# Performance work log

Measured on AMD Instinct MI355X. Metric: run time of the kernel, lower is better.

## Reference

```python
import jax, jax.numpy as jnp
import numpy as np

B, S, D, H = 2, 2048, 2048, 16
HD = D // H  # 128 head dim


def setup_inputs() -> dict:
    key = jax.random.key(0)
    k1, k2, k3 = jax.random.split(key, 3)
    x = jax.random.normal(k1, (B, S, D), dtype=jnp.float32)
    w_qkv = jax.random.normal(k2, (3 * D, D), dtype=jnp.float32) * 0.02
    w_out = jax.random.normal(k3, (D, D), dtype=jnp.float32) * 0.02
    # complex-like RoPE table: freqs_cis[s, j] = exp(i * s * theta^{-2j/hd})
    theta = 10000.0
    inv_freq = 1.0 / (theta ** (jnp.arange(0, HD, 2, dtype=jnp.float32) / HD))  # [HD/2]
    t = jnp.arange(S, dtype=jnp.float32)
    freqs = jnp.outer(t, inv_freq)  # [S, HD/2]
    return {"x": x, "w_qkv": w_qkv, "w_out": w_out,
            "freqs_cos": jnp.cos(freqs), "freqs_sin": jnp.sin(freqs)}


def _apply_rope(t, cos, sin):
    # t: [b, s, h, hd]; adjacent pairs treated as complex (real, imag)
    b, s, h, hd = t.shape
    tr = t.reshape(b, s, h, hd // 2, 2)
    re, im = tr[..., 0], tr[..., 1]
    c = cos[None, :, None, :]  # [1, s, 1, hd/2]
    sn = sin[None, :, None, :]
    out_re = re * c - im * sn
    out_im = re * sn + im * c
    return jnp.stack([out_re, out_im], axis=-1).reshape(b, s, h, hd)


def reference(x, w_qkv, w_out, freqs_cos, freqs_sin):
    b, s, d = x.shape
    qkv = x @ w_qkv.T  # [b, s, 3d]
    q, k, v = jnp.split(qkv, 3, axis=-1)
    q = q.reshape(b, s, H, HD)
    k = k.reshape(b, s, H, HD)
    v = v.reshape(b, s, H, HD)
    q = _apply_rope(q, freqs_cos, freqs_sin)
    k = _apply_rope(k, freqs_cos, freqs_sin)
    # causal SDPA
    scale = 1.0 / jnp.sqrt(jnp.asarray(HD, dtype=x.dtype))
    scores = jnp.einsum("bqhd,bkhd->bhqk", q, k) * scale  # [b, h, s, s]
    causal = jnp.tril(jnp.ones((s, s), dtype=bool))
    scores = jnp.where(causal[None, None], scores, jnp.finfo(scores.dtype).min)
    attn = jax.nn.softmax(scores, axis=-1)
    out = jnp.einsum("bhqk,bkhd->bqhd", attn, v).reshape(b, s, d)
    return out @ w_out.T
```

## Files before the change

### kernel.cpp

```cpp
#include <hip/hip_runtime.h>
#include <hip/hip_bf16.h>
#include <stdint.h>

#define S_ 2048
#define D_ 2048
#define H_ 16
#define HD_ 128

typedef __bf16 bf16x8 __attribute__((ext_vector_type(8)));
typedef float f32x4 __attribute__((ext_vector_type(4)));
typedef unsigned short ushort_t;
typedef ushort_t us4 __attribute__((ext_vector_type(4)));

__device__ __forceinline__ float bf2f(ushort_t u) {
  union { float f; uint32_t i; } x; x.i = ((uint32_t)u) << 16; return x.f;
}
__device__ __forceinline__ ushort_t f2bf(float f) {
  union { float f; uint32_t i; } x; x.f = f;
  uint32_t r = x.i + 0x7fffu + ((x.i >> 16) & 1u);
  return (ushort_t)(r >> 16);
}

__device__ __forceinline__ void async_copy16(const void* g, void* l) {
  __builtin_amdgcn_global_load_lds(
      (const __attribute__((address_space(1))) unsigned int*)g,
      (__attribute__((address_space(3))) unsigned int*)l, 16, 0, 0);
}

__device__ __forceinline__ void store_val(float* p, float v) { *p = v; }
__device__ __forceinline__ void store_val(ushort_t* p, float v) { *p = f2bf(v); }

__global__ __launch_bounds__(256) void cvt_f32_bf16(const float* __restrict__ in,
                                                    ushort_t* __restrict__ out,
                                                    int n4) {
  int i = blockIdx.x * 256 + threadIdx.x;
  if (i >= n4) return;
  const float4 v = ((const float4*)in)[i];
  us4 o;
  o.x = f2bf(v.x); o.y = f2bf(v.y); o.z = f2bf(v.z); o.w = f2bf(v.w);
  ((us4*)out)[i] = o;
}

__device__ __forceinline__ void stage_B32(const ushort_t* __restrict__ g, int K,
                                          ushort_t* l, int wave, int srow,
                                          int clog) {
  async_copy16(g + (size_t)srow * K + clog * 8, l + wave * 512);
  async_copy16(g + (size_t)(128 + srow) * K + clog * 8, l + 4096 + wave * 512);
}
__device__ __forceinline__ void stage_A32(const ushort_t* __restrict__ g, int K,
                                          ushort_t* l, int wave, int srow,
                                          int clog) {
  async_copy16(g + (size_t)srow * K + clog * 8, l + wave * 512);
}

#define MFMA_BF16(a, b, c) __builtin_amdgcn_mfma_f32_16x16x32_bf16(a, b, c, 0, 0, 0)

template <typename OutT>
__global__ __launch_bounds__(512, 4) void gemm_bt_occ2(const ushort_t* __restrict__ A,
                                                       const ushort_t* __restrict__ Bm,
                                                       OutT* __restrict__ C,
                                                       int M, int N, int K) {
  __shared__ __align__(16) ushort_t As[2][128 * 32];
  __shared__ __align__(16) ushort_t Bs[3][256 * 32];
  const int tid = threadIdx.x;
  const int wave = tid >> 6, lane = tid & 63;
  const int quad = lane >> 4, l16 = lane & 15;
  const int bm = blockIdx.y * 128, bn = blockIdx.x * 256;
  const int wm = (wave >> 2) * 64;
  const int wn = (wave & 3) * 64;
  const int srow = tid >> 2;
  const int clog = (tid & 3) ^ ((tid >> 3) & 3);
  const int ck = (quad ^ ((l16 >> 1) & 3)) * 8;

  const ushort_t* gA = A + (size_t)bm * K;
  const ushort_t* gB = Bm + (size_t)bn * K;
  const int NT = K >> 5;

  f32x4 acc[4][4] = {};

  const int arow0 = (wm + l16) * 32 + ck;
  const int brow0 = (wn + l16) * 32 + ck;

  stage_B32(gB, K, &Bs[0][0], wave, srow, clog);
  stage_A32(gA, K, &As[0][0], wave, srow, clog);
  stage_B32(gB + 32, K, &Bs[1][0], wave, srow, clog);
  stage_A32(gA + 32, K, &As[1][0], wave, srow, clog);
  asm volatile("s_waitcnt vmcnt(3)" ::: "memory");
  __builtin_amdgcn_sched_barrier(0);
  __builtin_amdgcn_s_barrier();

  int bc = 0;
  for (int ii = 0; ii < (NT >> 1); ++ii) {
    const int t = 2 * ii;
    const size_t k2 = (size_t)((t + 2 < NT) ? t + 2 : NT - 1) * 32;
    const size_t k3 = (size_t)((t + 3 < NT) ? t + 3 : NT - 1) * 32;
    const int bc1 = (bc + 1 < 3) ? bc + 1 : 0;
    const int bc2 = (bc + 2 < 3) ? bc + 2 : bc - 1;
    const ushort_t* At = &As[0][0];
    const ushort_t* At1 = &As[1][0];
    const ushort_t* Bt = &Bs[0][0] + bc * 8192;
    const ushort_t* Bt1 = &Bs[0][0] + bc1 * 8192;
    ushort_t* Bw2 = &Bs[0][0] + bc2 * 8192;
    ushort_t* Bw0 = &Bs[0][0] + bc * 8192;

    bf16x8 a4[4], b0[2], b1[2];

#pragma unroll
    for (int mi = 0; mi < 4; ++mi)
      a4[mi] = *(const bf16x8*)(At + arow0 + mi * 512);
#pragma unroll
    for (int ni = 0; ni < 2; ++ni)
      b0[ni] = *(const bf16x8*)(Bt + brow0 + ni * 512);
    stage_B32(gB + k2, K, Bw2, wave, srow, clog);
    __builtin_amdgcn_s_barrier();
    __builtin_amdgcn_s_setprio(1);
#pragma unroll
    for (int mi = 0; mi < 4; ++mi)
#pragma unroll
      for (int ni = 0; ni < 2; ++ni)
        acc[mi][ni] = MFMA_BF16(a4[mi], b0[ni], acc[mi][ni]);
    __builtin_amdgcn_s_setprio(0);
    __builtin_amdgcn_s_barrier();

#pragma unroll
    for (int ni = 0; ni < 2; ++ni)
      b1[ni] = *(const bf16x8*)(Bt + brow0 + (ni + 2) * 512);
    stage_A32(gA + k2, K, &As[0][0], wave, srow, clog);
    asm volatile("s_waitcnt vmcnt(3)" ::: "memory");
    __builtin_amdgcn_sched_barrier(0);
    __builtin_amdgcn_s_barrier();
    __builtin_amdgcn_s_setprio(1);
#pragma unroll
    for (int mi = 0; mi < 4; ++mi)
#pragma unroll
      for (int ni = 0; ni < 2; ++ni)
        acc[mi][ni + 2] = MFMA_BF16(a4[mi], b1[ni], acc[mi][ni + 2]);
    __builtin_amdgcn_s_setprio(0);
    __builtin_amdgcn_s_barrier();

#pragma unroll
    for (int mi = 0; mi < 4; ++mi)
      a4[mi] = *(const bf16x8*)(At1 + arow0 + mi * 512);
#pragma unroll
    for (int ni = 0; ni < 2; ++ni)
      b0[ni] = *(const bf16x8*)(Bt1 + brow0 + ni * 512);
    stage_B32(gB + k3, K, Bw0, wave, srow, clog);
    __builtin_amdgcn_s_barrier();
    __builtin_amdgcn_s_setprio(1);
#pragma unroll
    for (int mi = 0; mi < 4; ++mi)
#pragma unroll
      for (int ni = 0; ni < 2; ++ni)
        acc[mi][ni] = MFMA_BF16(a4[mi], b0[ni], acc[mi][ni]);
    __builtin_amdgcn_s_setprio(0);
    __builtin_amdgcn_s_barrier();

#pragma unroll
    for (int ni = 0; ni < 2; ++ni)
      b1[ni] = *(const bf16x8*)(Bt1 + brow0 + (ni + 2) * 512);
    stage_A32(gA + k3, K, &As[1][0], wave, srow, clog);
    asm volatile("s_waitcnt vmcnt(3)" ::: "memory");
    __builtin_amdgcn_sched_barrier(0);
    __builtin_amdgcn_s_barrier();
    __builtin_amdgcn_s_setprio(1);
#pragma unroll
    for (int mi = 0; mi < 4; ++mi)
#pragma unroll
      for (int ni = 0; ni < 2; ++ni)
        acc[mi][ni + 2] = MFMA_BF16(a4[mi], b1[ni], acc[mi][ni + 2]);
    __builtin_amdgcn_s_setprio(0);
    __builtin_amdgcn_s_barrier();
    __builtin_amdgcn_sched_barrier(0);

    bc = bc2;
  }

  asm volatile("s_waitcnt vmcnt(0)" ::: "memory");

#pragma unroll
  for (int mi = 0; mi < 4; ++mi)
#pragma unroll
    for (int ni = 0; ni < 4; ++ni)
#pragma unroll
      for (int r = 0; r < 4; ++r) {
        int row = bm + wm + mi * 16 + quad * 4 + r;
        int col = bn + wn + ni * 16 + l16;
        store_val(&C[(size_t)row * N + col], acc[mi][ni][r]);
      }
}

__device__ __forceinline__ void stage_half(const ushort_t* __restrict__ g, int K,
                                           ushort_t* l, int wave, int srow,
                                           int clog) {
#pragma unroll
  for (int i = 0; i < 2; ++i)
    async_copy16(g + (size_t)(i * 64 + srow) * K + clog * 8,
                 l + wave * 512 + i * 4096);
}

template <typename OutT>
__global__ __launch_bounds__(512, 2) void gemm_bt128_256(const ushort_t* __restrict__ A,
                                                         const ushort_t* __restrict__ Bm,
                                                         OutT* __restrict__ C,
                                                         int M, int N, int K) {
  __shared__ __align__(16) ushort_t As[2][128 * 64];
  __shared__ __align__(16) ushort_t Bs[2][256 * 64];
  const int tid = threadIdx.x;
  const int wave = tid >> 6, lane = tid & 63;
  const int quad = lane >> 4, l16 = lane & 15;
  const int bm = blockIdx.y * 128, bn = blockIdx.x * 256;
  const int wm = (wave >> 2) * 64;
  const int wn = (wave & 3) * 64;
  const int srow = tid >> 3;
  const int clog = (tid & 7) ^ (srow & 7);
  const int ck0 = (quad ^ (l16 & 7)) * 8;
  const int ck1 = ((4 + quad) ^ (l16 & 7)) * 8;

  const ushort_t* gA = A + (size_t)bm * K;
  const ushort_t* gB = Bm + (size_t)bn * K;
  const int NT = K >> 6;

  f32x4 acc[4][4] = {};

  const ushort_t* ArowE = &As[0][0] + (wm + l16) * 64;
  const ushort_t* BrowE = &Bs[0][0] + (wn + l16) * 64;
  const ushort_t* ArowO = &As[1][0] + (wm + l16) * 64;
  const ushort_t* BrowO = &Bs[1][0] + (wn + l16) * 64;

  stage_half(gA, K, &As[0][0], wave, srow, clog);
  stage_half(gB, K, &Bs[0][0], wave, srow, clog);
  stage_half(gB + (size_t)128 * K, K, &Bs[0][8192], wave, srow, clog);
  stage_half(gB + 64, K, &Bs[1][0], wave, srow, clog);
  stage_half(gB + (size_t)128 * K + 64, K, &Bs[1][8192], wave, srow, clog);
  asm volatile("s_waitcnt vmcnt(4)" ::: "memory");
  __builtin_amdgcn_sched_barrier(0);
  __builtin_amdgcn_s_barrier();

  for (int ii = 0; ii < (NT >> 1); ++ii) {
    const int t = 2 * ii;
    const int t2 = (t + 2 < NT) ? t + 2 : NT - 1;
    const int t3 = (t + 3 < NT) ? t + 3 : NT - 1;
    const size_t k1 = (size_t)(t + 1) * 64;
    const size_t k2 = (size_t)t2 * 64;
    const size_t k3 = (size_t)t3 * 64;

    bf16x8 a4[4][2], b01[2][2], b23[2][2];

#pragma unroll
    for (int mi = 0; mi < 2; ++mi) {
      a4[mi][0] = *(const bf16x8*)(ArowE + mi * 1024 + ck0);
      a4[mi][1] = *(const bf16x8*)(ArowE + mi * 1024 + ck1);
    }
#pragma unroll
    for (int ni = 0; ni < 2; ++ni) {
      b01[ni][0] = *(const bf16x8*)(BrowE + ni * 1024 + ck0);
      b01[ni][1] = *(const bf16x8*)(BrowE + ni * 1024 + ck1);
    }
    stage_half(gA + k1, K, &As[1][0], wave, srow, clog);
    __builtin_amdgcn_s_barrier();
    __builtin_amdgcn_s_setprio(1);
#pragma unroll
    for (int ks = 0; ks < 2; ++ks)
#pragma unroll
      for (int mi = 0; mi < 2; ++mi)
#pragma unroll
        for (int ni = 0; ni < 2; ++ni)
          acc[mi][ni] = MFMA_BF16(a4[mi][ks], b01[ni][ks], acc[mi][ni]);
    __builtin_amdgcn_s_setprio(0);
    __builtin_amdgcn_s_barrier();

#pragma unroll
    for (int ni = 0; ni < 2; ++ni) {
      b23[ni][0] = *(const bf16x8*)(BrowE + (ni + 2) * 1024 + ck0);
      b23[ni][1] = *(const bf16x8*)(BrowE + (ni + 2) * 1024 + ck1);
    }
    __builtin_amdgcn_s_barrier();
    __builtin_amdgcn_s_setprio(1);
#pragma unroll
    for (int ks = 0; ks < 2; ++ks)
#pragma unroll
      for (int mi = 0; mi < 2; ++mi)
#pragma unroll
        for (int ni = 0; ni < 2; ++ni)
          acc[mi][ni + 2] = MFMA_BF16(a4[mi][ks], b23[ni][ks], acc[mi][ni + 2]);
    __builtin_amdgcn_s_setprio(0);
    __builtin_amdgcn_s_barrier();

#pragma unroll
    for (int mi = 0; mi < 2; ++mi) {
      a4[mi + 2][0] = *(const bf16x8*)(ArowE + (mi + 2) * 1024 + ck0);
      a4[mi + 2][1] = *(const bf16x8*)(ArowE + (mi + 2) * 1024 + ck1);
    }
    stage_half(gB + k2, K, &Bs[0][0], wave, srow, clog);
    __builtin_amdgcn_s_barrier();
    __builtin_amdgcn_s_setprio(1);
#pragma unroll
    for (int ks = 0; ks < 2; ++ks)
#pragma unroll
      for (int mi = 0; mi < 2; ++mi)
#pragma unroll
        for (int ni = 0; ni < 2; ++ni)
          acc[mi + 2][ni] = MFMA_BF16(a4[mi + 2][ks], b01[ni][ks], acc[mi + 2][ni]);
    __builtin_amdgcn_s_setprio(0);
    __builtin_amdgcn_s_barrier();

    stage_half(gB + (size_t)128 * K + k2, K, &Bs[0][8192], wave, srow, clog);
    asm volatile("s_waitcnt vmcnt(4)" ::: "memory");
    __builtin_amdgcn_sched_barrier(0);
    __builtin_amdgcn_s_barrier();
    __builtin_amdgcn_s_setprio(1);
#pragma unroll
    for (int ks = 0; ks < 2; ++ks)
#pragma unroll
      for (int mi = 0; mi < 2; ++mi)
#pragma unroll
        for (int ni = 0; ni < 2; ++ni)
          acc[mi + 2][ni + 2] = MFMA_BF16(a4[mi + 2][ks], b23[ni][ks], acc[mi + 2][ni + 2]);
    __builtin_amdgcn_s_setprio(0);
    __builtin_amdgcn_s_barrier();

#pragma unroll
    for (int mi = 0; mi < 2; ++mi) {
      a4[mi][0] = *(const bf16x8*)(ArowO + mi * 1024 + ck0);
      a4[mi][1] = *(const bf16x8*)(ArowO + mi * 1024 + ck1);
    }
#pragma unroll
    for (int ni = 0; ni < 2; ++ni) {
      b01[ni][0] = *(const bf16x8*)(BrowO + ni * 1024 + ck0);
      b01[ni][1] = *(const bf16x8*)(BrowO + ni * 1024 + ck1);
    }
    stage_half(gA + k2, K, &As[0][0], wave, srow, clog);
    __builtin_amdgcn_s_barrier();
    __builtin_amdgcn_s_setprio(1);
#pragma unroll
    for (int ks = 0; ks < 2; ++ks)
#pragma unroll
      for (int mi = 0; mi < 2; ++mi)
#pragma unroll
        for (int ni = 0; ni < 2; ++ni)
          acc[mi][ni] = MFMA_BF16(a4[mi][ks], b01[ni][ks], acc[mi][ni]);
    __builtin_amdgcn_s_setprio(0);
    __builtin_amdgcn_s_barrier();

#pragma unroll
    for (int ni = 0; ni < 2; ++ni) {
      b23[ni][0] = *(const bf16x8*)(BrowO + (ni + 2) * 1024 + ck0);
      b23[ni][1] = *(const bf16x8*)(BrowO + (ni + 2) * 1024 + ck1);
    }
    __builtin_amdgcn_s_barrier();
    __builtin_amdgcn_s_setprio(1);
#pragma unroll
    for (int ks = 0; ks < 2; ++ks)
#pragma unroll
      for (int mi = 0; mi < 2; ++mi)
#pragma unroll
        for (int ni = 0; ni < 2; ++ni)
          acc[mi][ni + 2] = MFMA_BF16(a4[mi][ks], b23[ni][ks], acc[mi][ni + 2]);
    __builtin_amdgcn_s_setprio(0);
    __builtin_amdgcn_s_barrier();

#pragma unroll
    for (int mi = 0; mi < 2; ++mi) {
      a4[mi + 2][0] = *(const bf16x8*)(ArowO + (mi + 2) * 1024 + ck0);
      a4[mi + 2][1] = *(const bf16x8*)(ArowO + (mi + 2) * 1024 + ck1);
    }
    stage_half(gB + k3, K, &Bs[1][0], wave, srow, clog);
    __builtin_amdgcn_s_barrier();
    __builtin_amdgcn_s_setprio(1);
#pragma unroll
    for (int ks = 0; ks < 2; ++ks)
#pragma unroll
      for (int mi = 0; mi < 2; ++mi)
#pragma unroll
        for (int ni = 0; ni < 2; ++ni)
          acc[mi + 2][ni] = MFMA_BF16(a4[mi + 2][ks], b01[ni][ks], acc[mi + 2][ni]);
    __builtin_amdgcn_s_setprio(0);
    __builtin_amdgcn_s_barrier();

    stage_half(gB + (size_t)128 * K + k3, K, &Bs[1][8192], wave, srow, clog);
    asm volatile("s_waitcnt vmcnt(4)" ::: "memory");
    __builtin_amdgcn_sched_barrier(0);
    __builtin_amdgcn_s_barrier();
    __builtin_amdgcn_s_setprio(1);
#pragma unroll
    for (int ks = 0; ks < 2; ++ks)
#pragma unroll
      for (int mi = 0; mi < 2; ++mi)
#pragma unroll
        for (int ni = 0; ni < 2; ++ni)
          acc[mi + 2][ni + 2] = MFMA_BF16(a4[mi + 2][ks], b23[ni][ks], acc[mi + 2][ni + 2]);
    __builtin_amdgcn_s_setprio(0);
    __builtin_amdgcn_s_barrier();
    __builtin_amdgcn_sched_barrier(0);
  }

  asm volatile("s_waitcnt vmcnt(0)" ::: "memory");

#pragma unroll
  for (int mi = 0; mi < 4; ++mi)
#pragma unroll
    for (int ni = 0; ni < 4; ++ni)
#pragma unroll
      for (int r = 0; r < 4; ++r) {
        int row = bm + wm + mi * 16 + quad * 4 + r;
        int col = bn + wn + ni * 16 + l16;
        store_val(&C[(size_t)row * N + col], acc[mi][ni][r]);
      }
}

__global__ __launch_bounds__(256) void rope_k(ushort_t* __restrict__ qkv,
                                              const float* __restrict__ fc,
                                              const float* __restrict__ fs) {
  int idx = blockIdx.x * 256 + threadIdx.x;
  int i = idx & 63;
  int hh = (idx >> 6) & 15;
  int m = idx >> 10;
  int s = m & (S_ - 1);
  float c = fc[s * 64 + i], sn = fs[s * 64 + i];
  size_t off = (size_t)m * (3 * D_) + hh * HD_ + 2 * i;
#pragma unroll
  for (int part = 0; part < 2; ++part) {
    uint32_t* p = (uint32_t*)(qkv + off + part * D_);
    uint32_t v = *p;
    float re = bf2f((ushort_t)(v & 0xffffu));
    float im = bf2f((ushort_t)(v >> 16));
    float nr = re * c - im * sn;
    float ni = re * sn + im * c;
    *p = (uint32_t)f2bf(nr) | ((uint32_t)f2bf(ni) << 16);
  }
}

__global__ __launch_bounds__(256) void vt_prep(const ushort_t* __restrict__ qkv,
                                               ushort_t* __restrict__ VTg) {
  __shared__ __align__(16) ushort_t T[64 * 136];
  const int st = blockIdx.x, h = blockIdx.y, b = blockIdx.z;
  const int tid = threadIdx.x;
  const ushort_t* gV = qkv + (size_t)(b * S_ + st * 64) * (3 * D_) + 2 * D_ + h * HD_;
  {
    const int r = tid >> 2, cc = (tid & 3) * 32;
    const ushort_t* src = gV + (size_t)r * (3 * D_) + cc;
    uint4 a0 = ((const uint4*)src)[0];
    uint4 a1 = ((const uint4*)src)[1];
    uint4 a2 = ((const uint4*)src)[2];
    uint4 a3 = ((const uint4*)src)[3];
    ushort_t* dst = T + r * 136 + cc;
    ((uint4*)dst)[0] = a0; ((uint4*)dst)[1] = a1;
    ((uint4*)dst)[2] = a2; ((uint4*)dst)[3] = a3;
  }
  __syncthreads();
  const int d = tid >> 1, kh = (tid & 1) * 32;
  ushort_t buf[32];
#pragma unroll
  for (int j = 0; j < 32; ++j) buf[j] = T[(kh + j) * 136 + d];
  ushort_t* out = VTg + ((size_t)((b * H_ + h) * HD_ + d)) * S_ + st * 64 + kh;
  ((uint4*)out)[0] = *(const uint4*)(buf + 0);
  ((uint4*)out)[1] = *(const uint4*)(buf + 8);
  ((uint4*)out)[2] = *(const uint4*)(buf + 16);
  ((uint4*)out)[3] = *(const uint4*)(buf + 24);
}

#define SOFTMAX_C 12.0f

__global__ __launch_bounds__(256, 4) void attn_fwd(const ushort_t* __restrict__ qkv,
                                                   const ushort_t* __restrict__ VTg,
                                                   float* __restrict__ Oacc,
                                                   float* __restrict__ lsum_g) {
  __shared__ __align__(16) ushort_t Kl[64 * 128];
  __shared__ __align__(16) ushort_t VT[128 * 64];
  __shared__ __align__(16) ushort_t Pl[4 * 16 * 64];

  const int j = 79 - (int)blockIdx.x;
  int qt, c;
  if (j < 8)       { qt = j;                 c = 0; }
  else if (j < 24) { int t = j - 8;  qt = 8 + (t >> 1);  c = t & 1; }
  else if (j < 48) { int t = j - 24; qt = 16 + t / 3;    c = t % 3; }
  else             { int t = j - 48; qt = 24 + (t >> 2); c = t & 3; }
  const int h = blockIdx.y, b = blockIdx.z;
  const int kt0 = c * 8;
  const int kt_end = min(kt0 + 8, qt + 1);

  const int tid = threadIdx.x;
  const int wave = tid >> 6, lane = tid & 63;
  const int quad = lane >> 4, l16 = lane & 15;
  const float scale = 0.08838834764831845f;

  const int qg = qt * 64 + wave * 16 + l16;
  const ushort_t* qrow = qkv + (size_t)(b * S_ + qg) * (3 * D_) + h * HD_;
  bf16x8 qf[4];
#pragma unroll
  for (int cc = 0; cc < 4; ++cc)
    qf[cc] = *(const bf16x8*)(qrow + cc * 32 + quad * 8);

  f32x4 o[8] = {};
  float lsum[4] = {0.f, 0.f, 0.f, 0.f};
  const int q_row_base = qt * 64 + wave * 16 + quad * 4;
  ushort_t* Pw = Pl + wave * 16 * 64;

  const ushort_t* gK = qkv + (size_t)(b * S_) * (3 * D_) + D_ + h * HD_;
  const ushort_t* gVT = VTg + (size_t)(b * H_ + h) * HD_ * S_;

  const int krow_off = lane >> 4;
  const int kchunk = lane & 15;
  const int vrow_off = lane >> 3;
  const int vchunk = lane & 7;

  for (int kt = kt0; kt < kt_end; ++kt) {
    __syncthreads();
#pragma unroll
    for (int i = 0; i < 4; ++i) {
      int row = wave * 16 + i * 4 + krow_off;
      int lchunk = kchunk ^ (row & 15);
      async_copy16(gK + (size_t)(kt * 64 + row) * (3 * D_) + lchunk * 8,
                   Kl + (wave * 16 + i * 4) * 128);
    }
#pragma unroll
    for (int i = 0; i < 4; ++i) {
      int row = wave * 32 + i * 8 + vrow_off;
      int lchunk = vchunk ^ (row & 7);
      async_copy16(gVT + (size_t)row * S_ + kt * 64 + lchunk * 8,
                   VT + (wave * 32 + i * 8) * 64);
    }
    __syncthreads();

    const bool diag = (kt == qt);
#pragma unroll
    for (int g = 0; g < 4; ++g) {
      f32x4 s = {0.f, 0.f, 0.f, 0.f};
#pragma unroll
      for (int cc = 0; cc < 4; ++cc) {
        bf16x8 kf = *(const bf16x8*)(Kl + (g * 16 + l16) * 128 +
                                     (((cc * 4 + quad) ^ l16) * 8));
        s = __builtin_amdgcn_mfma_f32_16x16x32_bf16(qf[cc], kf, s, 0, 0, 0);
      }
      const int key = kt * 64 + g * 16 + l16;
#pragma unroll
      for (int r = 0; r < 4; ++r) {
        float e = __expf(s[r] * scale - SOFTMAX_C);
        float p = (!diag || key <= q_row_base + r) ? e : 0.f;
        lsum[r] += p;
        int prow = quad * 4 + r;
        int pcol = g * 16 + l16;
        Pw[prow * 64 + (((pcol >> 3) ^ (prow & 7)) * 8) + (pcol & 7)] = f2bf(p);
      }
    }
    bf16x8 pf0 = *(const bf16x8*)(Pw + l16 * 64 + ((quad ^ (l16 & 7)) * 8));
    bf16x8 pf1 = *(const bf16x8*)(Pw + l16 * 64 + (((4 + quad) ^ (l16 & 7)) * 8));
#pragma unroll
    for (int dc = 0; dc < 8; ++dc) {
      bf16x8 v0 = *(const bf16x8*)(VT + (dc * 16 + l16) * 64 +
                                   (((0 * 4 + quad) ^ (l16 & 7)) * 8));
      o[dc] = __builtin_amdgcn_mfma_f32_16x16x32_bf16(pf0, v0, o[dc], 0, 0, 0);
      bf16x8 v1 = *(const bf16x8*)(VT + (dc * 16 + l16) * 64 +
                                   (((1 * 4 + quad) ^ (l16 & 7)) * 8));
      o[dc] = __builtin_amdgcn_mfma_f32_16x16x32_bf16(pf1, v1, o[dc], 0, 0, 0);
    }
  }

#pragma unroll
  for (int r = 0; r < 4; ++r) {
    float l = lsum[r];
    l += __shfl_xor(l, 1, 64);
    l += __shfl_xor(l, 2, 64);
    l += __shfl_xor(l, 4, 64);
    l += __shfl_xor(l, 8, 64);
    size_t row = (size_t)(b * S_ + q_row_base + r);
    if (l16 == 0) unsafeAtomicAdd(&lsum_g[row * H_ + h], l);
#pragma unroll
    for (int dc = 0; dc < 8; ++dc)
      unsafeAtomicAdd(&Oacc[row * D_ + h * HD_ + dc * 16 + l16], o[dc][r]);
  }
}

__global__ __launch_bounds__(256) void combine(const float* __restrict__ Oacc,
                                               const float* __restrict__ lsum_g,
                                               ushort_t* __restrict__ attn) {
  int i = blockIdx.x * 256 + threadIdx.x;
  float4 v = ((const float4*)Oacc)[i];
  int flat = i * 4;
  int row = flat >> 11;
  int h = (flat >> 7) & 15;
  float inv = 1.0f / lsum_g[row * H_ + h];
  us4 o;
  o.x = f2bf(v.x * inv); o.y = f2bf(v.y * inv);
  o.z = f2bf(v.z * inv); o.w = f2bf(v.w * inv);
  ((us4*)attn)[i] = o;
}

extern "C" void kernel_launch(void* const* d_in, const int* in_sizes, int n_in,
                              void* d_out, int out_size, void* d_ws, size_t ws_size,
                              hipStream_t stream) {
  const float* x = (const float*)d_in[0];
  const float* w_qkv = (const float*)d_in[1];
  const float* w_out = (const float*)d_in[2];
  const float* fcos = (const float*)d_in[3];
  const float* fsin = (const float*)d_in[4];
  float* out = (float*)d_out;

  char* ws = (char*)d_ws;
  ushort_t* x_bf    = (ushort_t*)(ws + 0);
  ushort_t* wqkv_bf = (ushort_t*)(ws + 16777216);
  ushort_t* wout_bf = (ushort_t*)(ws + 41943040);
  ushort_t* qkv     = (ushort_t*)(ws + 50331648);
  ushort_t* attn    = (ushort_t*)(ws + 100663296);
  float* Oacc   = (float*)(ws + 0);
  float* lsum_g = (float*)(ws + 33554432);
  ushort_t* VTg = (ushort_t*)(ws + 100663296);

  cvt_f32_bf16<<<8192, 256, 0, stream>>>(x, x_bf, 2097152);
  cvt_f32_bf16<<<12288, 256, 0, stream>>>(w_qkv, wqkv_bf, 3145728);
  cvt_f32_bf16<<<4096, 256, 0, stream>>>(w_out, wout_bf, 1048576);

  gemm_bt_occ2<ushort_t><<<dim3(24, 32), 512, 0, stream>>>(x_bf, wqkv_bf, qkv,
                                                           4096, 6144, 2048);
  rope_k<<<16384, 256, 0, stream>>>(qkv, fcos, fsin);
  vt_prep<<<dim3(32, 16, 2), 256, 0, stream>>>(qkv, VTg);

  (void)hipMemsetAsync(Oacc, 0, 33554432, stream);
  (void)hipMemsetAsync(lsum_g, 0, 262144, stream);

  attn_fwd<<<dim3(80, 16, 2), 256, 0, stream>>>(qkv, VTg, Oacc, lsum_g);
  combine<<<8192, 256, 0, stream>>>(Oacc, lsum_g, attn);

  gemm_bt128_256<float><<<dim3(8, 32), 512, 0, stream>>>(attn, wout_bf, out,
                                                         4096, 2048, 2048);
}
```

Baseline: 446.0 us.

## Replace QKV projection GEMM with 256x256 tile, BK=64 double-buffered kernel

The QKV projection GEMM moves from a 128x256 tile with K-step 32 and a triple-buffered B stage to a 256x256 tile with K-step 64, double-buffered A and B, and 8x4 accumulator fragments per wave. Each loaded byte is reused across more output, so global and LDS traffic per FLOP drops and there are fewer barriers per unit of K. In exchange, LDS use rises to about 128KB per block and register pressure grows, occupancy falls to 2 blocks per CU, and the grid shrinks to 384 blocks, which can underfill 256 CUs.

```diff
diff --git a/kernel.cpp b/kernel.cpp
--- a/kernel.cpp
+++ b/kernel.cpp
@@ -41,144 +41,221 @@
   ((us4*)out)[i] = o;
 }
 
-__device__ __forceinline__ void stage_B32(const ushort_t* __restrict__ g, int K,
-                                          ushort_t* l, int wave, int srow,
-                                          int clog) {
-  async_copy16(g + (size_t)srow * K + clog * 8, l + wave * 512);
-  async_copy16(g + (size_t)(128 + srow) * K + clog * 8, l + 4096 + wave * 512);
-}
-__device__ __forceinline__ void stage_A32(const ushort_t* __restrict__ g, int K,
-                                          ushort_t* l, int wave, int srow,
-                                          int clog) {
-  async_copy16(g + (size_t)srow * K + clog * 8, l + wave * 512);
+__device__ __forceinline__ void stage_half(const ushort_t* __restrict__ g, int K,
+                                           ushort_t* l, int wave, int srow,
+                                           int clog) {
+#pragma unroll
+  for (int i = 0; i < 2; ++i)
+    async_copy16(g + (size_t)(i * 64 + srow) * K + clog * 8,
+                 l + wave * 512 + i * 4096);
 }
 
 #define MFMA_BF16(a, b, c) __builtin_amdgcn_mfma_f32_16x16x32_bf16(a, b, c, 0, 0, 0)
 
 template <typename OutT>
-__global__ __launch_bounds__(512, 4) void gemm_bt_occ2(const ushort_t* __restrict__ A,
-                                                       const ushort_t* __restrict__ Bm,
-                                                       OutT* __restrict__ C,
-                                                       int M, int N, int K) {
-  __shared__ __align__(16) ushort_t As[2][128 * 32];
-  __shared__ __align__(16) ushort_t Bs[3][256 * 32];
+__global__ __launch_bounds__(512, 2) void gemm_bt256(const ushort_t* __restrict__ A,
+                                                     const ushort_t* __restrict__ Bm,
+                                                     OutT* __restrict__ C,
+                                                     int M, int N, int K) {
+  __shared__ __align__(16) ushort_t As[2][256 * 64];
+  __shared__ __align__(16) ushort_t Bs[2][256 * 64];
   const int tid = threadIdx.x;
   const int wave = tid >> 6, lane = tid & 63;
   const int quad = lane >> 4, l16 = lane & 15;
-  const int bm = blockIdx.y * 128, bn = blockIdx.x * 256;
-  const int wm = (wave >> 2) * 64;
+  const int bm = blockIdx.y * 256, bn = blockIdx.x * 256;
+  const int wm = (wave >> 2) * 128;
   const int wn = (wave & 3) * 64;
-  const int srow = tid >> 2;
-  const int clog = (tid & 3) ^ ((tid >> 3) & 3);
-  const int ck = (quad ^ ((l16 >> 1) & 3)) * 8;
+  const int srow = tid >> 3;
+  const int clog = (tid & 7) ^ (srow & 7);
+  const int ck0 = (quad ^ (l16 & 7)) * 8;
+  const int ck1 = ((4 + quad) ^ (l16 & 7)) * 8;
 
   const ushort_t* gA = A + (size_t)bm * K;
   const ushort_t* gB = Bm + (size_t)bn * K;
-  const int NT = K >> 5;
-
-  f32x4 acc[4][4] = {};
-
-  const int arow0 = (wm + l16) * 32 + ck;
-  const int brow0 = (wn + l16) * 32 + ck;
-
-  stage_B32(gB, K, &Bs[0][0], wave, srow, clog);
-  stage_A32(gA, K, &As[0][0], wave, srow, clog);
-  stage_B32(gB + 32, K, &Bs[1][0], wave, srow, clog);
-  stage_A32(gA + 32, K, &As[1][0], wave, srow, clog);
-  asm volatile("s_waitcnt vmcnt(3)" ::: "memory");
+  const int NT = K >> 6;
+
+  f32x4 acc[8][4] = {};
+
+  const ushort_t* ArowE = &As[0][0] + (wm + l16) * 64;
+  const ushort_t* BrowE = &Bs[0][0] + (wn + l16) * 64;
+  const ushort_t* ArowO = &As[1][0] + (wm + l16) * 64;
+  const ushort_t* BrowO = &Bs[1][0] + (wn + l16) * 64;
+
+  stage_half(gB, K, &Bs[0][0], wave, srow, clog);
+  stage_half(gB + (size_t)128 * K, K, &Bs[0][8192], wave, srow, clog);
+  stage_half(gA, K, &As[0][0], wave, srow, clog);
+  stage_half(gA + (size_t)128 * K, K, &As[0][8192], wave, srow, clog);
+  stage_half(gB + 64, K, &Bs[1][0], wave, srow, clog);
+  stage_half(gB + (size_t)128 * K + 64, K, &Bs[1][8192], wave, srow, clog);
+  stage_half(gA + 64, K, &As[1][0], wave, srow, clog);
+  stage_half(gA + (size_t)128 * K + 64, K, &As[1][8192], wave, srow, clog);
+  asm volatile("s_waitcnt vmcnt(8)" ::: "memory");
   __builtin_amdgcn_sched_barrier(0);
   __builtin_amdgcn_s_barrier();
 
-  int bc = 0;
   for (int ii = 0; ii < (NT >> 1); ++ii) {
     const int t = 2 * ii;
-    const size_t k2 = (size_t)((t + 2 < NT) ? t + 2 : NT - 1) * 32;
-    const size_t k3 = (size_t)((t + 3 < NT) ? t + 3 : NT - 1) * 32;
-    const int bc1 = (bc + 1 < 3) ? bc + 1 : 0;
-    const int bc2 = (bc + 2 < 3) ? bc + 2 : bc - 1;
-    const ushort_t* At = &As[0][0];
-    const ushort_t* At1 = &As[1][0];
-    const ushort_t* Bt = &Bs[0][0] + bc * 8192;
-    const ushort_t* Bt1 = &Bs[0][0] + bc1 * 8192;
-    ushort_t* Bw2 = &Bs[0][0] + bc2 * 8192;
-    ushort_t* Bw0 = &Bs[0][0] + bc * 8192;
-
-    bf16x8 a4[4], b0[2], b1[2];
-
-#pragma unroll
-    for (int mi = 0; mi < 4; ++mi)
-      a4[mi] = *(const bf16x8*)(At + arow0 + mi * 512);
-#pragma unroll
-    for (int ni = 0; ni < 2; ++ni)
-      b0[ni] = *(const bf16x8*)(Bt + brow0 + ni * 512);
-    stage_B32(gB + k2, K, Bw2, wave, srow, clog);
-    __builtin_amdgcn_s_barrier();
-    __builtin_amdgcn_s_setprio(1);
-#pragma unroll
-    for (int mi = 0; mi < 4; ++mi)
-#pragma unroll
-      for (int ni = 0; ni < 2; ++ni)
-        acc[mi][ni] = MFMA_BF16(a4[mi], b0[ni], acc[mi][ni]);
-    __builtin_amdgcn_s_setprio(0);
-    __builtin_amdgcn_s_barrier();
-
-#pragma unroll
-    for (int ni = 0; ni < 2; ++ni)
-      b1[ni] = *(const bf16x8*)(Bt + brow0 + (ni + 2) * 512);
-    stage_A32(gA + k2, K, &As[0][0], wave, srow, clog);
-    asm volatile("s_waitcnt vmcnt(3)" ::: "memory");
+    const int t2 = (t + 2 < NT) ? t + 2 : NT - 1;
+    const int t3 = (t + 3 < NT) ? t + 3 : NT - 1;
+    const size_t k2 = (size_t)t2 * 64;
+    const size_t k3 = (size_t)t3 * 64;
+
+    bf16x8 a4[4][2], b01[2][2], b23[2][2];
+
+#pragma unroll
+    for (int mi = 0; mi < 4; ++mi) {
+      a4[mi][0] = *(const bf16x8*)(ArowE + mi * 1024 + ck0);
+      a4[mi][1] = *(const bf16x8*)(ArowE + mi * 1024 + ck1);
+    }
+#pragma unroll
+    for (int ni = 0; ni < 2; ++ni) {
+      b01[ni][0] = *(const bf16x8*)(BrowE + ni * 1024 + ck0);
+      b01[ni][1] = *(const bf16x8*)(BrowE + ni * 1024 + ck1);
+    }
+    __builtin_amdgcn_s_barrier();
+    __builtin_amdgcn_s_setprio(1);
+#pragma unroll
+    for (int ks = 0; ks < 2; ++ks)
+#pragma unroll
+      for (int mi = 0; mi < 4; ++mi)
+#pragma unroll
+        for (int ni = 0; ni < 2; ++ni)
+          acc[mi][ni] = MFMA_BF16(a4[mi][ks], b01[ni][ks], acc[mi][ni]);
+    __builtin_amdgcn_s_setprio(0);
+    __builtin_amdgcn_s_barrier();
+
+#pragma unroll
+    for (int ni = 0; ni < 2; ++ni) {
+      b23[ni][0] = *(const bf16x8*)(BrowE + (ni + 2) * 1024 + ck0);
+      b23[ni][1] = *(const bf16x8*)(BrowE + (ni + 2) * 1024 + ck1);
+    }
+    __builtin_amdgcn_s_barrier();
+    __builtin_amdgcn_s_setprio(1);
+#pragma unroll
+    for (int ks = 0; ks < 2; ++ks)
+#pragma unroll
+      for (int mi = 0; mi < 4; ++mi)
+#pragma unroll
+        for (int ni = 0; ni < 2; ++ni)
+          acc[mi][ni + 2] = MFMA_BF16(a4[mi][ks], b23[ni][ks], acc[mi][ni + 2]);
+    __builtin_amdgcn_s_setprio(0);
+    __builtin_amdgcn_s_barrier();
+
+#pragma unroll
+    for (int mi = 0; mi < 4; ++mi) {
+      a4[mi][0] = *(const bf16x8*)(ArowE + (mi + 4) * 1024 + ck0);
+      a4[mi][1] = *(const bf16x8*)(ArowE + (mi + 4) * 1024 + ck1);
+    }
+    stage_half(gB + k2, K, &Bs[0][0], wave, srow, clog);
+    stage_half(gB + (size_t)128 * K + k2, K, &Bs[0][8192], wave, srow, clog);
+    __builtin_amdgcn_s_barrier();
+    __builtin_amdgcn_s_setprio(1);
+#pragma unroll
+    for (int ks = 0; ks < 2; ++ks)
+#pragma unroll
+      for (int mi = 0; mi < 4; ++mi)
+#pragma unroll
+        for (int ni = 0; ni < 2; ++ni)
+          acc[mi + 4][ni] = MFMA_BF16(a4[mi][ks], b01[ni][ks], acc[mi + 4][ni]);
+    __builtin_amdgcn_s_setprio(0);
+    __builtin_amdgcn_s_barrier();
+
+    stage_half(gA + k2, K, &As[0][0], wave, srow, clog);
+    stage_half(gA + (size_t)128 * K + k2, K, &As[0][8192], wave, srow, clog);
+    asm volatile("s_waitcnt vmcnt(8)" ::: "memory");
     __builtin_amdgcn_sched_barrier(0);
     __builtin_amdgcn_s_barrier();
     __builtin_amdgcn_s_setprio(1);
 #pragma unroll
-    for (int mi = 0; mi < 4; ++mi)
-#pragma unroll
-      for (int ni = 0; ni < 2; ++ni)
-        acc[mi][ni + 2] = MFMA_BF16(a4[mi], b1[ni], acc[mi][ni + 2]);
-    __builtin_amdgcn_s_setprio(0);
-    __builtin_amdgcn_s_barrier();
-
-#pragma unroll
-    for (int mi = 0; mi < 4; ++mi)
-      a4[mi] = *(const bf16x8*)(At1 + arow0 + mi * 512);
-#pragma unroll
-    for (int ni = 0; ni < 2; ++ni)
-      b0[ni] = *(const bf16x8*)(Bt1 + brow0 + ni * 512);
-    stage_B32(gB + k3, K, Bw0, wave, srow, clog);
-    __builtin_amdgcn_s_barrier();
-    __builtin_amdgcn_s_setprio(1);
-#pragma unroll
-    for (int mi = 0; mi < 4; ++mi)
-#pragma unroll
-      for (int ni = 0; ni < 2; ++ni)
-        acc[mi][ni] = MFMA_BF16(a4[mi], b0[ni], acc[mi][ni]);
-    __builtin_amdgcn_s_setprio(0);
-    __builtin_amdgcn_s_barrier();
-
-#pragma unroll
-    for (int ni = 0; ni < 2; ++ni)
-      b1[ni] = *(const bf16x8*)(Bt1 + brow0 + (ni + 2) * 512);
-    stage_A32(gA + k3, K, &As[1][0], wave, srow, clog);
-    asm volatile("s_waitcnt vmcnt(3)" ::: "memory");
+    for (int ks = 0; ks < 2; ++ks)
+#pragma unroll
+      for (int mi = 0; mi < 4; ++mi)
+#pragma unroll
+        for (int ni = 0; ni < 2; ++ni)
+          acc[mi + 4][ni + 2] = MFMA_BF16(a4[mi][ks], b23[ni][ks], acc[mi + 4][ni + 2]);
+    __builtin_amdgcn_s_setprio(0);
+    __builtin_amdgcn_s_barrier();
+
+#pragma unroll
+    for (int mi = 0; mi < 4; ++mi) {
+      a4[mi][0] = *(const bf16x8*)(ArowO + mi * 1024 + ck0);
+      a4[mi][1] = *(const bf16x8*)(ArowO + mi * 1024 + ck1);
+    }
+#pragma unroll
+    for (int ni = 0; ni < 2; ++ni) {
+      b01[ni][0] = *(const bf16x8*)(BrowO + ni * 1024 + ck0);
+      b01[ni][1] = *(const bf16x8*)(BrowO + ni * 1024 + ck1);
+    }
+    __builtin_amdgcn_s_barrier();
+    __builtin_amdgcn_s_setprio(1);
+#pragma unroll
+    for (int ks = 0; ks < 2; ++ks)
+#pragma unroll
+      for (int mi = 0; mi < 4; ++mi)
+#pragma unroll
+        for (int ni = 0; ni < 2; ++ni)
+          acc[mi][ni] = MFMA_BF16(a4[mi][ks], b01[ni][ks], acc[mi][ni]);
+    __builtin_amdgcn_s_setprio(0);
+    __builtin_amdgcn_s_barrier();
+
+#pragma unroll
+    for (int ni = 0; ni < 2; ++ni) {
+      b23[ni][0] = *(const bf16x8*)(BrowO + (ni + 2) * 1024 + ck0);
+      b23[ni][1] = *(const bf16x8*)(BrowO + (ni + 2) * 1024 + ck1);
+    }
+    __builtin_amdgcn_s_barrier();
+    __builtin_amdgcn_s_setprio(1);
+#pragma unroll
+    for (int ks = 0; ks < 2; ++ks)
+#pragma unroll
+      for (int mi = 0; mi < 4; ++mi)
+#pragma unroll
+        for (int ni = 0; ni < 2; ++ni)
+          acc[mi][ni + 2] = MFMA_BF16(a4[mi][ks], b23[ni][ks], acc[mi][ni + 2]);
+    __builtin_amdgcn_s_setprio(0);
+    __builtin_amdgcn_s_barrier();
+
+#pragma unroll
+    for (int mi = 0; mi < 4; ++mi) {
+      a4[mi][0] = *(const bf16x8*)(ArowO + (mi + 4) * 1024 + ck0);
+      a4[mi][1] = *(const bf16x8*)(ArowO + (mi + 4) * 1024 + ck1);
+    }
+    stage_half(gB + k3, K, &Bs[1][0], wave, srow, clog);
+    stage_half(gB + (size_t)128 * K + k3, K, &Bs[1][8192], wave, srow, clog);
+    __builtin_amdgcn_s_barrier();
+    __builtin_amdgcn_s_setprio(1);
+#pragma unroll
+    for (int ks = 0; ks < 2; ++ks)
+#pragma unroll
+      for (int mi = 0; mi < 4; ++mi)
+#pragma unroll
+        for (int ni = 0; ni < 2; ++ni)
+          acc[mi + 4][ni] = MFMA_BF16(a4[mi][ks], b01[ni][ks], acc[mi + 4][ni]);
+    __builtin_amdgcn_s_setprio(0);
+    __builtin_amdgcn_s_barrier();
+
+    stage_half(gA + k3, K, &As[1][0], wave, srow, clog);
+    stage_half(gA + (size_t)128 * K + k3, K, &As[1][8192], wave, srow, clog);
+    asm volatile("s_waitcnt vmcnt(8)" ::: "memory");
     __builtin_amdgcn_sched_barrier(0);
     __builtin_amdgcn_s_barrier();
     __builtin_amdgcn_s_setprio(1);
 #pragma unroll
-    for (int mi = 0; mi < 4; ++mi)
-#pragma unroll
-      for (int ni = 0; ni < 2; ++ni)
-        acc[mi][ni + 2] = MFMA_BF16(a4[mi], b1[ni], acc[mi][ni + 2]);
+    for (int ks = 0; ks < 2; ++ks)
+#pragma unroll
+      for (int mi = 0; mi < 4; ++mi)
+#pragma unroll
+        for (int ni = 0; ni < 2; ++ni)
+          acc[mi + 4][ni + 2] = MFMA_BF16(a4[mi][ks], b23[ni][ks], acc[mi + 4][ni + 2]);
     __builtin_amdgcn_s_setprio(0);
     __builtin_amdgcn_s_barrier();
     __builtin_amdgcn_sched_barrier(0);
-
-    bc = bc2;
   }
 
   asm volatile("s_waitcnt vmcnt(0)" ::: "memory");
 
 #pragma unroll
-  for (int mi = 0; mi < 4; ++mi)
+  for (int mi = 0; mi < 8; ++mi)
 #pragma unroll
     for (int ni = 0; ni < 4; ++ni)
 #pragma unroll
@@ -187,15 +264,6 @@
         int col = bn + wn + ni * 16 + l16;
         store_val(&C[(size_t)row * N + col], acc[mi][ni][r]);
       }
-}
-
-__device__ __forceinline__ void stage_half(const ushort_t* __restrict__ g, int K,
-                                           ushort_t* l, int wave, int srow,
-                                           int clog) {
-#pragma unroll
-  for (int i = 0; i < 2; ++i)
-    async_copy16(g + (size_t)(i * 64 + srow) * K + clog * 8,
-                 l + wave * 512 + i * 4096);
 }
 
 template <typename OutT>
@@ -610,8 +678,8 @@
   cvt_f32_bf16<<<12288, 256, 0, stream>>>(w_qkv, wqkv_bf, 3145728);
   cvt_f32_bf16<<<4096, 256, 0, stream>>>(w_out, wout_bf, 1048576);
 
-  gemm_bt_occ2<ushort_t><<<dim3(24, 32), 512, 0, stream>>>(x_bf, wqkv_bf, qkv,
-                                                           4096, 6144, 2048);
+  gemm_bt256<ushort_t><<<dim3(24, 16), 512, 0, stream>>>(x_bf, wqkv_bf, qkv,
+                                                         4096, 6144, 2048);
   rope_k<<<16384, 256, 0, stream>>>(qkv, fcos, fsin);
   vt_prep<<<dim3(32, 16, 2), 256, 0, stream>>>(qkv, VTg);
 
```

Result: no change. 442.0 us (-0.9%).
